# Kernel optimization log

Hardware: AMD Instinct MI355X
Metric: run time of the kernel (lower is better)

Reference implementation:

```python
import jax, jax.numpy as jnp
import numpy as np

N = 50000      # nodes
E = 400000     # edges per relation
R = 3          # edge types
D = 128        # input_dim == hidden_dim
H = 8          # attention heads
Dh = D // H    # per-head dim (16)
OUT = 1        # output logits
NEG_SLOPE = 0.2
LN_EPS = 1e-5


def setup_inputs() -> dict:
    key = jax.random.key(0)
    ks = jax.random.split(key, 20)
    s = 0.05
    f32 = jnp.float32
    return {
        "feat": jax.random.normal(ks[0], (N, D), f32),
        "edge_src": jax.random.randint(ks[1], (R, E), 0, N, dtype=jnp.int32),
        "edge_dst": jax.random.randint(ks[2], (R, E), 0, N, dtype=jnp.int32),
        # conv1: per-relation GATConv params (W, attn_l, attn_r, bias)
        "W1": jax.random.normal(ks[3], (R, D, H * Dh), f32) * s,
        "al1": jax.random.normal(ks[4], (R, H, Dh), f32) * s,
        "ar1": jax.random.normal(ks[5], (R, H, Dh), f32) * s,
        "b1": jnp.zeros((R, H * Dh), f32),
        # conv2
        "W2": jax.random.normal(ks[6], (R, D, H * Dh), f32) * s,
        "al2": jax.random.normal(ks[7], (R, H, Dh), f32) * s,
        "ar2": jax.random.normal(ks[8], (R, H, Dh), f32) * s,
        "b2": jnp.zeros((R, H * Dh), f32),
        # LayerNorm
        "ln_g": jnp.ones((D,), f32),
        "ln_b": jnp.zeros((D,), f32),
        # classifier MLP (dropout inactive at eval)
        "Wc1": jax.random.normal(ks[9], (D, D), f32) * s,
        "bc1": jnp.zeros((D,), f32),
        "Wc2": jax.random.normal(ks[10], (D, OUT), f32) * s,
        "bc2": jnp.zeros((OUT,), f32),
    }


def _gat(x, src, dst, W, al, ar, b):
    """DGL GATConv on one relation: x [N,Din] -> [N, H*Dh]."""
    h = (x @ W).reshape(N, H, Dh)                       # projected feats
    el = (h * al).sum(-1)                               # [N,H] src attn term
    er = (h * ar).sum(-1)                               # [N,H] dst attn term
    e = jax.nn.leaky_relu(el[src] + er[dst], NEG_SLOPE)  # [E,H]
    # edge-softmax over incoming edges per dst node, per head
    m = jax.ops.segment_max(e, dst, num_segments=N)     # [N,H]
    ex = jnp.exp(e - m[dst])
    denom = jax.ops.segment_sum(ex, dst, num_segments=N)
    alpha = ex / denom[dst]                             # [E,H]
    msg = alpha[:, :, None] * h[src]                    # [E,H,Dh]
    out = jax.ops.segment_sum(msg, dst, num_segments=N)  # [N,H,Dh]
    return out.reshape(N, H * Dh) + b


def _hetero(x, edge_src, edge_dst, W, al, ar, b):
    out = jnp.zeros((N, H * Dh), x.dtype)
    for r in range(R):  # small fixed relation count
        out = out + _gat(x, edge_src[r], edge_dst[r], W[r], al[r], ar[r], b[r])
    return out


def reference(feat, edge_src, edge_dst, W1, al1, ar1, b1, W2, al2, ar2, b2,
              ln_g, ln_b, Wc1, bc1, Wc2, bc2):
    h1 = jax.nn.relu(_hetero(feat, edge_src, edge_dst, W1, al1, ar1, b1))
    h2 = _hetero(h1, edge_src, edge_dst, W2, al2, ar2, b2)
    h = h2 + h1
    mu = h.mean(-1, keepdims=True)
    var = ((h - mu) ** 2).mean(-1, keepdims=True)
    h = (h - mu) * jax.lax.rsqrt(var + LN_EPS) * ln_g + ln_b
    h = jax.nn.relu(h @ Wc1 + bc1)
    return h @ Wc2 + bc2
```

## Files before the change

kernel.cpp:

```cpp
#include <hip/hip_runtime.h>
#include <math.h>

#define NN 50000
#define NNP 50001
#define NE 400000
#define NREL 3
#define CAP 32
#define EQ 300000
#define SENT 50000

typedef __bf16 bf16x8 __attribute__((ext_vector_type(8)));
typedef float floatx4 __attribute__((ext_vector_type(4)));

__device__ __forceinline__ unsigned short f2bf(float f) {
  unsigned int u = __float_as_uint(f);
  return (unsigned short)((u + 0x7fffu + ((u >> 16) & 1u)) >> 16);
}
__device__ __forceinline__ float bflo(unsigned int u) {
  return __uint_as_float(u << 16);
}
__device__ __forceinline__ float bfhi(unsigned int u) {
  return __uint_as_float(u & 0xffff0000u);
}

__global__ __launch_bounds__(256) void prep_wt(
    const float* __restrict__ W1, const float* __restrict__ W2,
    const float* __restrict__ Wc1, unsigned short* __restrict__ Wt) {
  int mat = blockIdx.x >> 3, slab = blockIdx.x & 7;
  const float* Wsrc = mat < 3 ? W1 + mat * 16384
                    : (mat < 6 ? W2 + (mat - 3) * 16384 : Wc1);
  unsigned short* dst = Wt + (size_t)mat * 144 * 128;
  int k0 = slab * 16;
#pragma unroll
  for (int i = 0; i < 8; ++i) {
    int idx = i * 256 + threadIdx.x;
    int k = k0 + (idx >> 7), nn = idx & 127;
    dst[nn * 128 + k] = f2bf(Wsrc[k * 128 + nn]);
  }
}

__global__ __launch_bounds__(256) void prep_attn(
    const float* __restrict__ W1, const float* __restrict__ W2,
    const float* __restrict__ al1, const float* __restrict__ ar1,
    const float* __restrict__ al2, const float* __restrict__ ar2,
    unsigned short* __restrict__ Wt, float* __restrict__ el) {
  int mat = blockIdx.x;
  if (mat < 3 && threadIdx.x < 8)
    el[(size_t)mat * NNP * 8 + (size_t)NN * 8 + threadIdx.x] = -1e30f;
  const float* Wsrc = mat < 3 ? W1 + mat * 16384 : W2 + (mat - 3) * 16384;
  const float* alp = mat < 3 ? al1 + mat * 128 : al2 + (mat - 3) * 128;
  const float* arp = mat < 3 ? ar1 + mat * 128 : ar2 + (mat - 3) * 128;
  unsigned short* dst = Wt + (size_t)mat * 144 * 128;
#pragma unroll
  for (int i = 0; i < 8; ++i) {
    int j = i * 256 + threadIdx.x;
    int half = j >> 10, jj = j & 1023;
    int k = jj >> 3, h = jj & 7;
    const float* av = half ? arp : alp;
    float s = 0.f;
#pragma unroll
    for (int d = 0; d < 16; ++d) s += Wsrc[k * 128 + h * 16 + d] * av[h * 16 + d];
    dst[(128 + half * 8 + h) * 128 + k] = f2bf(s);
  }
}

__global__ __launch_bounds__(256) void gemm3_attn_mfma(
    const float* __restrict__ X, const unsigned short* __restrict__ Wt,
    unsigned short* __restrict__ hp, float* __restrict__ el,
    float* __restrict__ er, int n) {
  __shared__ unsigned short Xs[64 * 136];
  __shared__ unsigned short Ws[144 * 136];
  int t = threadIdx.x;
  int rowbase = blockIdx.x * 64;

  const float4* X4 = (const float4*)X;
#pragma unroll
  for (int i = 0; i < 8; ++i) {
    int v = t + i * 256;
    int row = v >> 5, k4 = (v & 31) * 4;
    float4 x = make_float4(0.f, 0.f, 0.f, 0.f);
    if (rowbase + row < n) x = X4[(size_t)(rowbase + row) * 32 + (v & 31)];
    ushort4 p;
    p.x = f2bf(x.x); p.y = f2bf(x.y); p.z = f2bf(x.z); p.w = f2bf(x.w);
    *(ushort4*)&Xs[row * 136 + k4] = p;
  }

  int lane = t & 63, wave = t >> 6;
  int quad = lane >> 4, l = lane & 15;

  for (int r = 0; r < NREL; ++r) {
    __syncthreads();
    const uint4* WtR = (const uint4*)(Wt + (size_t)r * 144 * 128);
#pragma unroll
    for (int i = 0; i < 9; ++i) {
      int v = t + i * 256;
      ((uint4*)Ws)[(v >> 4) * 17 + (v & 15)] = WtR[v];
    }
    __syncthreads();

    floatx4 acc[9];
#pragma unroll
    for (int i = 0; i < 9; ++i) acc[i] = floatx4{0.f, 0.f, 0.f, 0.f};
#pragma unroll
    for (int ks = 0; ks < 4; ++ks) {
      bf16x8 a = *(const bf16x8*)&Xs[(wave * 16 + l) * 136 + ks * 32 + quad * 8];
#pragma unroll
      for (int nt = 0; nt < 9; ++nt) {
        bf16x8 b = *(const bf16x8*)&Ws[(nt * 16 + l) * 136 + ks * 32 + quad * 8];
        acc[nt] = __builtin_amdgcn_mfma_f32_16x16x32_bf16(a, b, acc[nt], 0, 0, 0);
      }
    }

    unsigned short* hpR = hp + (size_t)r * NNP * 128;
    float* elR = el + (size_t)r * NNP * 8;
    float* erR = er + (size_t)r * NN * 8;
    int r0 = rowbase + wave * 16 + quad * 4;
#pragma unroll
    for (int reg = 0; reg < 4; ++reg) {
      int row = r0 + reg;
      if (row < n) {
#pragma unroll
        for (int nt = 0; nt < 8; ++nt)
          hpR[(size_t)row * 128 + nt * 16 + l] = f2bf(acc[nt][reg]);
        if (l < 8) elR[row * 8 + l] = acc[8][reg];
        else       erR[row * 8 + (l - 8)] = acc[8][reg];
      }
    }
  }
}

__global__ __launch_bounds__(256) void gemm_head_mfma(
    const float* __restrict__ X, const unsigned short* __restrict__ Wt,
    const float* __restrict__ bc1, const float* __restrict__ wc2,
    const float* __restrict__ bc2, float* __restrict__ out, int n) {
  __shared__ unsigned short Xs[64 * 136];
  __shared__ unsigned short Ws[128 * 136];
  int t = threadIdx.x;
  int rowbase = blockIdx.x * 64;

  const float4* X4 = (const float4*)X;
#pragma unroll
  for (int i = 0; i < 8; ++i) {
    int v = t + i * 256;
    int row = v >> 5, k4 = (v & 31) * 4;
    float4 x = make_float4(0.f, 0.f, 0.f, 0.f);
    if (rowbase + row < n) x = X4[(size_t)(rowbase + row) * 32 + (v & 31)];
    ushort4 p;
    p.x = f2bf(x.x); p.y = f2bf(x.y); p.z = f2bf(x.z); p.w = f2bf(x.w);
    *(ushort4*)&Xs[row * 136 + k4] = p;
  }
  const uint4* WtR = (const uint4*)Wt;
#pragma unroll
  for (int i = 0; i < 8; ++i) {
    int v = t + i * 256;
    ((uint4*)Ws)[(v >> 4) * 17 + (v & 15)] = WtR[v];
  }
  __syncthreads();

  int lane = t & 63, wave = t >> 6;
  int quad = lane >> 4, l = lane & 15;

  floatx4 acc[8];
#pragma unroll
  for (int i = 0; i < 8; ++i) acc[i] = floatx4{0.f, 0.f, 0.f, 0.f};
#pragma unroll
  for (int ks = 0; ks < 4; ++ks) {
    bf16x8 a = *(const bf16x8*)&Xs[(wave * 16 + l) * 136 + ks * 32 + quad * 8];
#pragma unroll
    for (int nt = 0; nt < 8; ++nt) {
      bf16x8 b = *(const bf16x8*)&Ws[(nt * 16 + l) * 136 + ks * 32 + quad * 8];
      acc[nt] = __builtin_amdgcn_mfma_f32_16x16x32_bf16(a, b, acc[nt], 0, 0, 0);
    }
  }

  float bv[8], wv[8];
#pragma unroll
  for (int nt = 0; nt < 8; ++nt) {
    bv[nt] = bc1[nt * 16 + l];
    wv[nt] = wc2[nt * 16 + l];
  }
  int r0 = rowbase + wave * 16 + quad * 4;
#pragma unroll
  for (int reg = 0; reg < 4; ++reg) {
    float s = 0.f;
#pragma unroll
    for (int nt = 0; nt < 8; ++nt)
      s += fmaxf(acc[nt][reg] + bv[nt], 0.f) * wv[nt];
    s += __shfl_xor(s, 1); s += __shfl_xor(s, 2);
    s += __shfl_xor(s, 4); s += __shfl_xor(s, 8);
    int row = r0 + reg;
    if (l == 0 && row < n) out[row] = s + bc2[0];
  }
}

__global__ __launch_bounds__(256) void fill_ell(
    uint4* __restrict__ colE4, int* __restrict__ cnt) {
  int t = blockIdx.x * 256 + threadIdx.x;
  const unsigned int S2 = (unsigned)SENT | ((unsigned)SENT << 16);
  if (t < NREL * NN * CAP / 8)
    colE4[t] = make_uint4(S2, S2, S2, S2);
  if (t < NREL * NN) cnt[t] = 0;
}

__global__ __launch_bounds__(256) void build_ell(
    const int* __restrict__ esrc, const int* __restrict__ edst,
    int* __restrict__ cnt, unsigned short* __restrict__ colE) {
  int t = blockIdx.x * 256 + threadIdx.x;
  if (t >= EQ) return;
  int d[4], s[4], r[4];
#pragma unroll
  for (int k = 0; k < 4; ++k) {
    int tt = t + k * EQ;
    r[k] = tt / NE;
    d[k] = edst[tt];
    s[k] = esrc[tt];
  }
#pragma unroll
  for (int k = 0; k < 4; ++k) {
    int pos = atomicAdd(&cnt[r[k] * NN + d[k]], 1);
    colE[(((size_t)r[k] * NN + d[k]) << 5) + pos] = (unsigned short)s[k];
  }
}

__global__ __launch_bounds__(256) void gather_all(
    const int* __restrict__ cnt, const unsigned short* __restrict__ colE,
    const float* __restrict__ el, const float* __restrict__ er,
    const unsigned short* __restrict__ hp, const float* __restrict__ b,
    float* __restrict__ h1, const float* __restrict__ g,
    const float* __restrict__ beta, int mode) {
  int wid = (blockIdx.x * 256 + threadIdx.x) >> 6;
  int lane = threadIdx.x & 63;
  if (wid >= NN) return;
  int p = lane >> 5;
  int q = lane & 31;
  int head = q >> 2;
  float ax = 0.f, ay = 0.f, az = 0.f, aw = 0.f;
#pragma unroll
  for (int r = 0; r < NREL; ++r) {
    int deg = cnt[r * NN + wid];
    if (deg <= 0) continue;
    const unsigned short* cl = colE + (((size_t)r * NN + wid) << 5);
    const float* elr = el + (size_t)r * NNP * 8;
    const unsigned short* hpr = hp + (size_t)r * NNP * 128;
    float er_d = er[(size_t)r * NN * 8 + wid * 8 + head];
    int degp = (deg + 3) & ~3;
    float den = 0.f, f0 = 0.f, f1 = 0.f, f2 = 0.f, f3 = 0.f;
    for (int i = 0; i < degp; i += 4) {
      ushort4 c4 = *(const ushort4*)&cl[i];
      int s0 = p ? c4.z : c4.x;
      int s1 = p ? c4.w : c4.y;
      float e0 = elr[s0 * 8 + head] + er_d;
      float e1 = elr[s1 * 8 + head] + er_d;
      uint2 u0 = *(const uint2*)&hpr[(size_t)s0 * 128 + q * 4];
      uint2 u1 = *(const uint2*)&hpr[(size_t)s1 * 128 + q * 4];
      e0 = (e0 > 0.f) ? e0 : 0.2f * e0;
      e1 = (e1 > 0.f) ? e1 : 0.2f * e1;
      float x0 = __expf(e0);
      float x1 = __expf(e1);
      den += x0 + x1;
      f0 += x0 * bflo(u0.x) + x1 * bflo(u1.x);
      f1 += x0 * bfhi(u0.x) + x1 * bfhi(u1.x);
      f2 += x0 * bflo(u0.y) + x1 * bflo(u1.y);
      f3 += x0 * bfhi(u0.y) + x1 * bfhi(u1.y);
    }
    den += __shfl_xor(den, 32);
    float inv = 1.f / den;
    ax += f0 * inv; ay += f1 * inv; az += f2 * inv; aw += f3 * inv;
  }
  ax += __shfl_xor(ax, 32); ay += __shfl_xor(ay, 32);
  az += __shfl_xor(az, 32); aw += __shfl_xor(aw, 32);

  int c = q * 4;
  float4 b0 = *(const float4*)&b[c];
  float4 bb1 = *(const float4*)&b[128 + c];
  float4 bb2 = *(const float4*)&b[256 + c];
  float vx = ax + b0.x + bb1.x + bb2.x;
  float vy = ay + b0.y + bb1.y + bb2.y;
  float vz = az + b0.z + bb1.z + bb2.z;
  float vw = aw + b0.w + bb1.w + bb2.w;
  float4* hptr = (float4*)&h1[(size_t)wid * 128 + c];
  if (mode == 0) {
    if (p == 0)
      *hptr = make_float4(fmaxf(vx, 0.f), fmaxf(vy, 0.f),
                          fmaxf(vz, 0.f), fmaxf(vw, 0.f));
  } else {
    float4 r1 = *hptr;
    vx += r1.x; vy += r1.y; vz += r1.z; vw += r1.w;
    float s = vx + vy + vz + vw;
    s += __shfl_xor(s, 1); s += __shfl_xor(s, 2);
    s += __shfl_xor(s, 4); s += __shfl_xor(s, 8); s += __shfl_xor(s, 16);
    float mu = s * (1.f / 128.f);
    float dx = vx - mu, dy = vy - mu, dz = vz - mu, dw = vw - mu;
    float sq = dx * dx + dy * dy + dz * dz + dw * dw;
    sq += __shfl_xor(sq, 1); sq += __shfl_xor(sq, 2);
    sq += __shfl_xor(sq, 4); sq += __shfl_xor(sq, 8); sq += __shfl_xor(sq, 16);
    float rstd = rsqrtf(sq * (1.f / 128.f) + 1e-5f);
    float4 gv = *(const float4*)&g[c];
    float4 bv = *(const float4*)&beta[c];
    if (p == 0)
      *hptr = make_float4(dx * rstd * gv.x + bv.x, dy * rstd * gv.y + bv.y,
                          dz * rstd * gv.z + bv.z, dw * rstd * gv.w + bv.w);
  }
}

extern "C" void kernel_launch(void* const* d_in, const int* in_sizes, int n_in,
                              void* d_out, int out_size, void* d_ws, size_t ws_size,
                              hipStream_t stream) {
  const float* feat = (const float*)d_in[0];
  const int* esrc = (const int*)d_in[1];
  const int* edst = (const int*)d_in[2];
  const float* W1 = (const float*)d_in[3];
  const float* al1 = (const float*)d_in[4];
  const float* ar1 = (const float*)d_in[5];
  const float* b1 = (const float*)d_in[6];
  const float* W2 = (const float*)d_in[7];
  const float* al2 = (const float*)d_in[8];
  const float* ar2 = (const float*)d_in[9];
  const float* b2 = (const float*)d_in[10];
  const float* lng = (const float*)d_in[11];
  const float* lnb = (const float*)d_in[12];
  const float* Wc1 = (const float*)d_in[13];
  const float* bc1 = (const float*)d_in[14];
  const float* Wc2 = (const float*)d_in[15];
  const float* bc2 = (const float*)d_in[16];
  float* out = (float*)d_out;

  unsigned short* hp = (unsigned short*)d_ws;
  float* el = (float*)(hp + (size_t)3 * NNP * 128);
  float* er = el + (size_t)3 * NNP * 8;
  float* h1 = er + (size_t)3 * NN * 8;
  int* cnt = (int*)(h1 + (size_t)NN * 128);
  unsigned short* colE = (unsigned short*)(cnt + NREL * NN);
  unsigned short* Wt = colE + (size_t)NREL * NN * CAP;

  const int gemm_grid = (NN + 63) / 64;
  const int edge_grid = (EQ + 255) / 256;
  const int fill_grid = (NREL * NN * CAP / 8 + 255) / 256;
  const int gg_grid = (NN * 64) / 256;

  prep_wt<<<56, 256, 0, stream>>>(W1, W2, Wc1, Wt);
  prep_attn<<<6, 256, 0, stream>>>(W1, W2, al1, ar1, al2, ar2, Wt, el);

  fill_ell<<<fill_grid, 256, 0, stream>>>((uint4*)colE, cnt);
  build_ell<<<edge_grid, 256, 0, stream>>>(esrc, edst, cnt, colE);

  gemm3_attn_mfma<<<gemm_grid, 256, 0, stream>>>(feat, Wt, hp, el, er, NN);
  gather_all<<<gg_grid, 256, 0, stream>>>(cnt, colE, el, er, hp, b1,
                                          h1, nullptr, nullptr, 0);
  gemm3_attn_mfma<<<gemm_grid, 256, 0, stream>>>(
      h1, Wt + (size_t)3 * 144 * 128, hp, el, er, NN);
  gather_all<<<gg_grid, 256, 0, stream>>>(cnt, colE, el, er, hp, b2,
                                          h1, lng, lnb, 1);
  gemm_head_mfma<<<gemm_grid, 256, 0, stream>>>(
      h1, Wt + (size_t)6 * 144 * 128, bc1, Wc2, bc2, out, NN);
}
```

Before: 406.1 us.

## Bin edges by relation and destination range before building ELL adjacency

Replaces the single scatter kernel that built the ELL adjacency with a two-pass binning scheme. The first pass counts edges per (relation, destination block of 2048 nodes) bin in shared memory and writes packed dst/src pairs into per-bin segments. The second pass then does the per-node atomic insertion bin by bin, so atomics and colE writes hit a localized region that can stay in cache. This adds an extra kernel launch and an extra pass over the edges through an intermediate buffer. It also relies on a fixed per-bin capacity that holds for uniformly random destinations.

Measured after the change: 424.1 us. +4.4%, slower.

```diff
diff --git a/kernel.cpp b/kernel.cpp
--- a/kernel.cpp
+++ b/kernel.cpp
@@ -6,8 +6,11 @@
 #define NE 400000
 #define NREL 3
 #define CAP 32
-#define EQ 300000
 #define SENT 50000
+#define BINS_PER_REL 25
+#define TOT_BINS 75
+#define SEGCAP 17408
+#define BPB 9
 
 typedef __bf16 bf16x8 __attribute__((ext_vector_type(8)));
 typedef float floatx4 __attribute__((ext_vector_type(4)));
@@ -194,31 +197,69 @@
 }
 
 __global__ __launch_bounds__(256) void fill_ell(
-    uint4* __restrict__ colE4, int* __restrict__ cnt) {
+    uint4* __restrict__ colE4, int* __restrict__ cnt, int* __restrict__ binCnt) {
   int t = blockIdx.x * 256 + threadIdx.x;
   const unsigned int S2 = (unsigned)SENT | ((unsigned)SENT << 16);
   if (t < NREL * NN * CAP / 8)
     colE4[t] = make_uint4(S2, S2, S2, S2);
   if (t < NREL * NN) cnt[t] = 0;
-}
-
-__global__ __launch_bounds__(256) void build_ell(
+  if (t < TOT_BINS) binCnt[t] = 0;
+}
+
+__global__ __launch_bounds__(256) void bin_a(
     const int* __restrict__ esrc, const int* __restrict__ edst,
+    int* __restrict__ binCnt, unsigned int* __restrict__ binBuf) {
+  __shared__ int hist[TOT_BINS];
+  __shared__ int base[TOT_BINS];
+  int t = threadIdx.x;
+  if (t < TOT_BINS) hist[t] = 0;
+  __syncthreads();
+  int e0 = blockIdx.x * 2048;
+  unsigned int pk[8];
+  int bn[8];
+  bool val[8];
+#pragma unroll
+  for (int i = 0; i < 8; ++i) {
+    int e = e0 + i * 256 + t;
+    val[i] = e < NREL * NE;
+    int ee = val[i] ? e : NREL * NE - 1;
+    int rel = ee / NE;
+    int d = edst[ee], s = esrc[ee];
+    pk[i] = ((unsigned)d << 16) | (unsigned)s;
+    bn[i] = rel * BINS_PER_REL + (d >> 11);
+    if (val[i]) atomicAdd(&hist[bn[i]], 1);
+  }
+  __syncthreads();
+  if (t < TOT_BINS) {
+    base[t] = atomicAdd(&binCnt[t], hist[t]);
+    hist[t] = 0;
+  }
+  __syncthreads();
+#pragma unroll
+  for (int i = 0; i < 8; ++i) {
+    if (val[i]) {
+      int p = base[bn[i]] + atomicAdd(&hist[bn[i]], 1);
+      binBuf[(size_t)bn[i] * SEGCAP + p] = pk[i];
+    }
+  }
+}
+
+__global__ __launch_bounds__(256) void bin_b(
+    const int* __restrict__ binCnt, const unsigned int* __restrict__ binBuf,
     int* __restrict__ cnt, unsigned short* __restrict__ colE) {
-  int t = blockIdx.x * 256 + threadIdx.x;
-  if (t >= EQ) return;
-  int d[4], s[4], r[4];
-#pragma unroll
-  for (int k = 0; k < 4; ++k) {
-    int tt = t + k * EQ;
-    r[k] = tt / NE;
-    d[k] = edst[tt];
-    s[k] = esrc[tt];
-  }
-#pragma unroll
-  for (int k = 0; k < 4; ++k) {
-    int pos = atomicAdd(&cnt[r[k] * NN + d[k]], 1);
-    colE[(((size_t)r[k] * NN + d[k]) << 5) + pos] = (unsigned short)s[k];
+  int bin = blockIdx.x / BPB, chunk = blockIdx.x % BPB;
+  int n = binCnt[bin];
+  int rel = bin / BINS_PER_REL;
+  const unsigned int* seg = binBuf + (size_t)bin * SEGCAP;
+#pragma unroll
+  for (int i = 0; i < 8; ++i) {
+    int idx = chunk * 2048 + i * 256 + threadIdx.x;
+    if (idx < n) {
+      unsigned int pk = seg[idx];
+      int d = pk >> 16, s = pk & 0xffff;
+      int pos = atomicAdd(&cnt[rel * NN + d], 1);
+      colE[(((size_t)rel * NN + d) << 5) + pos] = (unsigned short)s;
+    }
   }
 }
 
@@ -330,19 +371,23 @@
   float* er = el + (size_t)3 * NNP * 8;
   float* h1 = er + (size_t)3 * NN * 8;
   int* cnt = (int*)(h1 + (size_t)NN * 128);
-  unsigned short* colE = (unsigned short*)(cnt + NREL * NN);
-  unsigned short* Wt = colE + (size_t)NREL * NN * CAP;
+  int* binCnt = cnt + NREL * NN;
+  unsigned short* colE = (unsigned short*)(binCnt + TOT_BINS);
+  unsigned int* binBuf = (unsigned int*)(colE + (size_t)NREL * NN * CAP);
+  unsigned short* Wt = (unsigned short*)(binBuf + (size_t)TOT_BINS * SEGCAP);
 
   const int gemm_grid = (NN + 63) / 64;
-  const int edge_grid = (EQ + 255) / 256;
+  const int ba_grid = (NREL * NE + 2047) / 2048;
+  const int bb_grid = TOT_BINS * BPB;
   const int fill_grid = (NREL * NN * CAP / 8 + 255) / 256;
   const int gg_grid = (NN * 64) / 256;
 
   prep_wt<<<56, 256, 0, stream>>>(W1, W2, Wc1, Wt);
   prep_attn<<<6, 256, 0, stream>>>(W1, W2, al1, ar1, al2, ar2, Wt, el);
 
-  fill_ell<<<fill_grid, 256, 0, stream>>>((uint4*)colE, cnt);
-  build_ell<<<edge_grid, 256, 0, stream>>>(esrc, edst, cnt, colE);
+  fill_ell<<<fill_grid, 256, 0, stream>>>((uint4*)colE, cnt, binCnt);
+  bin_a<<<ba_grid, 256, 0, stream>>>(esrc, edst, binCnt, binBuf);
+  bin_b<<<bb_grid, 256, 0, stream>>>(binCnt, binBuf, cnt, colE);
 
   gemm3_attn_mfma<<<gemm_grid, 256, 0, stream>>>(feat, Wt, hp, el, er, NN);
   gather_all<<<gg_grid, 256, 0, stream>>>(cnt, colE, el, er, hp, b1,
```
